# Kernel tuning notes

Hardware: AMD Instinct MI355X
Metric: run time of the kernel (lower is better)

The kernel has to match this reference:

```python
import jax, jax.numpy as jnp
import numpy as np

PAST = 12
FUTURE = 12
INPUT_SIZE = 256
OUTPUT_SIZE = FUTURE * INPUT_SIZE  # 3072


def setup_inputs() -> dict:
    key = jax.random.key(0)
    k_inp, k_w, k_b = jax.random.split(key, 3)
    inp = jax.random.normal(k_inp, (64, 288, INPUT_SIZE), dtype=jnp.float32)
    fan_in = INPUT_SIZE * PAST
    bound = 1.0 / np.sqrt(fan_in)
    # torch nn.Linear init: U(-1/sqrt(fan_in), 1/sqrt(fan_in)); W is (out, in)
    W = jax.random.uniform(k_w, (OUTPUT_SIZE, fan_in), minval=-bound, maxval=bound, dtype=jnp.float32)
    b = jax.random.uniform(k_b, (OUTPUT_SIZE,), minval=-bound, maxval=bound, dtype=jnp.float32)
    return {"inp": inp, "W": W, "b": b}


def reference(inp, W, b):
    batch, length, dim = inp.shape
    n_win = length - PAST  # number of sliding windows (torch loop count)
    # Gather all overlapping windows at once: (batch, n_win, PAST, dim)
    idx = jnp.arange(n_win)[:, None] + jnp.arange(PAST)[None, :]
    windows = inp[:, idx, :].reshape(batch, n_win, PAST * dim)
    # One batched GEMM replaces n_win tiny Linear calls: x @ W.T + b
    out = jnp.einsum('bnk,ok->bno', windows, W) + b
    return out.reshape(batch, -1, FUTURE, dim)
```

## Files before the change

### kernel.cpp

```cpp
#include <hip/hip_runtime.h>
#include <hip/hip_bf16.h>

#define BATCH   64
#define LEN     288
#define DIM     256
#define PAST    12
#define NWIN    (LEN - PAST)
#define M_DIM   (BATCH * NWIN)
#define K_DIM   (PAST * DIM)
#define N_DIM   3072

#define BM 256
#define BN 256
#define BK 64
#define NTILE   (K_DIM / BK)
#define NITER   (NTILE / 2)

#define GRID_N   12
#define BULK_WG  768
#define TAIL_M0  16384
#define TAIL_QN  24
#define TAIL_WG  240

typedef __attribute__((ext_vector_type(8))) short bh8;
typedef __attribute__((ext_vector_type(4))) float f32x4;

__device__ __forceinline__ void llds16(const void* g, void* l) {
    __builtin_amdgcn_global_load_lds(
        (const __attribute__((address_space(1))) unsigned int*)g,
        (__attribute__((address_space(3))) unsigned int*)l,
        16, 0, 0);
}

__global__ void cvt_f32_bf16(const float* __restrict__ in,
                             __hip_bfloat16* __restrict__ out, int n8) {
    int i = blockIdx.x * blockDim.x + threadIdx.x;
    if (i >= n8) return;
    const float4* p = (const float4*)in;
    float4 a = p[2 * i], b = p[2 * i + 1];
    union { __hip_bfloat16 h[8]; int4 v; } u;
    u.h[0] = __float2bfloat16(a.x); u.h[1] = __float2bfloat16(a.y);
    u.h[2] = __float2bfloat16(a.z); u.h[3] = __float2bfloat16(a.w);
    u.h[4] = __float2bfloat16(b.x); u.h[5] = __float2bfloat16(b.y);
    u.h[6] = __float2bfloat16(b.z); u.h[7] = __float2bfloat16(b.w);
    ((int4*)out)[i] = u.v;
}

#define PH_MID  __builtin_amdgcn_sched_barrier(0); __builtin_amdgcn_s_barrier(); \
                __builtin_amdgcn_sched_barrier(0); __builtin_amdgcn_s_setprio(1);
#define PH_END  __builtin_amdgcn_s_setprio(0); __builtin_amdgcn_sched_barrier(0); \
                __builtin_amdgcn_s_barrier(); __builtin_amdgcn_sched_barrier(0);
#define PH_END_VM(N) __builtin_amdgcn_s_setprio(0); __builtin_amdgcn_sched_barrier(0); \
                asm volatile("s_waitcnt vmcnt(" #N ")" ::: "memory"); \
                __builtin_amdgcn_s_barrier(); __builtin_amdgcn_sched_barrier(0);

#define LDS_A(buf) (smem + (buf) * 65536)
#define LDS_B(buf) (smem + (buf) * 65536 + 32768)

#define RD_A4(buf, MB) { \
    const char* _b = LDS_A(buf) + aRowB; \
    _Pragma("unroll") for (int mi = 0; mi < 4; ++mi) { \
        a0[mi][0] = *(const bh8*)(_b + (MB + mi) * 2048 + kOff0); \
        a0[mi][1] = *(const bh8*)(_b + (MB + mi) * 2048 + kOff1); \
    } }
#define RD_B2(buf, dst, NB) { \
    const char* _b = LDS_B(buf) + bRowB; \
    _Pragma("unroll") for (int ni = 0; ni < 2; ++ni) { \
        dst[ni][0] = *(const bh8*)(_b + (NB + ni) * 2048 + kOff0); \
        dst[ni][1] = *(const bh8*)(_b + (NB + ni) * 2048 + kOff1); \
    } }
#define MFMA_Q(MB, NB, BB) \
    _Pragma("unroll") for (int mi = 0; mi < 4; ++mi) \
    _Pragma("unroll") for (int ni = 0; ni < 2; ++ni) { \
        acc[MB + mi][NB + ni] = __builtin_amdgcn_mfma_f32_16x16x32_bf16( \
            a0[mi][0], BB[ni][0], acc[MB + mi][NB + ni], 0, 0, 0); \
        acc[MB + mi][NB + ni] = __builtin_amdgcn_mfma_f32_16x16x32_bf16( \
            a0[mi][1], BB[ni][1], acc[MB + mi][NB + ni], 0, 0, 0); \
    }
#define STG_A1(buf, kt, q) \
    llds16(Ag + aSrc[q] + (kt) * 64, LDS_A(buf) + (q) * 8192 + wOff);
#define STG_B1(buf, kt, u) \
    llds16(Wg + bSrc[u] + (kt) * 64, LDS_B(buf) + (u) * 8192 + wOff);

__global__ __launch_bounds__(512, 2)
void gemm_bulk(const __hip_bfloat16* __restrict__ Ag,
               const __hip_bfloat16* __restrict__ Wg,
               const float* __restrict__ bias,
               float* __restrict__ C)
{
    extern __shared__ char smem[];

    const int tid = threadIdx.x;
    const int wgid = (blockIdx.x & 7) * (BULK_WG / 8) + (blockIdx.x >> 3);
    const int bm = wgid / GRID_N;
    const int bn = wgid - bm * GRID_N;
    const int tile_m = bm * BM;
    const int tile_n = bn * BN;

    const int rd  = tid >> 3;
    const int chs = (((tid & 7) ^ (rd & 7)) * 8);
    int aSrc[4], bSrc[4];
#pragma unroll
    for (int rb = 0; rb < 4; ++rb) {
        int m  = tile_m + rb * 64 + rd;
        int bq = m / NWIN;
        int wq = m - bq * NWIN;
        aSrc[rb] = (bq * LEN + wq) * DIM + chs;
        bSrc[rb] = (tile_n + rb * 64 + rd) * K_DIM + chs;
    }

    const int wave = tid >> 6, lane = tid & 63;
    const int wm = wave >> 2, wn = wave & 3;
    const int fr = lane & 15, kg = lane >> 4;
    const int sw    = (fr & 7) << 4;
    const int kOff0 = (kg * 16) ^ sw;
    const int kOff1 = kOff0 ^ 64;
    const int aRowB = (wm * 128 + fr) * 128;
    const int bRowB = (wn * 64 + fr) * 128;
    const int wOff  = wave * 1024;

    bh8 a0[4][2], fb0[2][2], fb1[2][2];
    f32x4 acc[8][4] = {};

    STG_A1(0, 0, 0); STG_A1(0, 0, 1); STG_A1(0, 0, 2); STG_A1(0, 0, 3);
    STG_B1(0, 0, 0); STG_B1(0, 0, 1); STG_B1(0, 0, 2); STG_B1(0, 0, 3);
    STG_A1(1, 1, 0); STG_A1(1, 1, 2);
    STG_B1(1, 1, 0); STG_B1(1, 1, 1);
    STG_A1(1, 1, 1); STG_A1(1, 1, 3);
    asm volatile("s_waitcnt vmcnt(6)" ::: "memory");
    __builtin_amdgcn_s_barrier();
    __builtin_amdgcn_sched_barrier(0);

#pragma unroll 1
    for (int it = 0; it < NITER; ++it) {
        const int b = 2 * it + 1;
        int c = 2 * it + 2; if (c >= NTILE) c = NTILE - 2;
        int d = 2 * it + 3; if (d >= NTILE) d = NTILE - 1;

        RD_B2(0, fb0, 0); RD_A4(0, 0);
        STG_B1(1, b, 2); STG_B1(1, b, 3);
        PH_MID; MFMA_Q(0, 0, fb0); PH_END;

        RD_B2(0, fb1, 2);
        STG_A1(0, c, 0); STG_A1(0, c, 2);
        PH_MID; MFMA_Q(0, 2, fb1); PH_END;

        RD_A4(0, 4);
        STG_B1(0, c, 0); STG_B1(0, c, 1);
        PH_MID; MFMA_Q(4, 2, fb1); PH_END;

        STG_A1(0, c, 1); STG_A1(0, c, 3);
        PH_MID; MFMA_Q(4, 0, fb0); PH_END_VM(6);

        RD_B2(1, fb0, 0); RD_A4(1, 0);
        STG_B1(0, c, 2); STG_B1(0, c, 3);
        PH_MID; MFMA_Q(0, 0, fb0); PH_END;

        RD_B2(1, fb1, 2);
        STG_A1(1, d, 0); STG_A1(1, d, 2);
        PH_MID; MFMA_Q(0, 2, fb1); PH_END;

        RD_A4(1, 4);
        STG_B1(1, d, 0); STG_B1(1, d, 1);
        PH_MID; MFMA_Q(4, 2, fb1); PH_END;

        STG_A1(1, d, 1); STG_A1(1, d, 3);
        PH_MID; MFMA_Q(4, 0, fb0); PH_END_VM(6);
    }

    float bv[4];
    const float* bp = bias + tile_n + wn * 64 + fr;
#pragma unroll
    for (int ni = 0; ni < 4; ++ni) bv[ni] = bp[ni * 16];

    const int r0 = (lane >> 4) * 4;
#pragma unroll
    for (int mi = 0; mi < 8; ++mi) {
#pragma unroll
        for (int j = 0; j < 4; ++j) {
            long m = tile_m + wm * 128 + mi * 16 + r0 + j;
            float* crow = C + m * (long)N_DIM + tile_n + wn * 64 + fr;
#pragma unroll
            for (int ni = 0; ni < 4; ++ni)
                __builtin_nontemporal_store(acc[mi][ni][j] + bv[ni], &crow[ni * 16]);
        }
    }
}

#define TLDS_A(buf) (smem + (buf) * 32768)
#define TLDS_B(buf) (smem + (buf) * 32768 + 16384)

#define T_RD(buf) { \
    const char* _bb = TLDS_B(buf) + bRowB; \
    _Pragma("unroll") for (int ni = 0; ni < 2; ++ni) { \
        fb0[ni][0] = *(const bh8*)(_bb + ni * 2048 + kOff0); \
        fb0[ni][1] = *(const bh8*)(_bb + ni * 2048 + kOff1); \
    } \
    const char* _a = TLDS_A(buf) + aRowB; \
    _Pragma("unroll") for (int mi = 0; mi < 4; ++mi) { \
        a0[mi][0] = *(const bh8*)(_a + mi * 2048 + kOff0); \
        a0[mi][1] = *(const bh8*)(_a + mi * 2048 + kOff1); \
    } }
#define T_MFMA(MB) \
    _Pragma("unroll") for (int mi = 0; mi < 2; ++mi) \
    _Pragma("unroll") for (int ni = 0; ni < 2; ++ni) { \
        acc[MB + mi][ni] = __builtin_amdgcn_mfma_f32_16x16x32_bf16( \
            a0[MB + mi][0], fb0[ni][0], acc[MB + mi][ni], 0, 0, 0); \
        acc[MB + mi][ni] = __builtin_amdgcn_mfma_f32_16x16x32_bf16( \
            a0[MB + mi][1], fb0[ni][1], acc[MB + mi][ni], 0, 0, 0); \
    }
#define T_STG_A(buf, kt, u) \
    llds16(Ag + aSrc[u] + (kt) * 64, TLDS_A(buf) + (u) * 8192 + wOff);
#define T_STG_B(buf, kt, u) \
    llds16(Wg + bSrc[u] + (kt) * 64, TLDS_B(buf) + (u) * 8192 + wOff);

__global__ __launch_bounds__(512, 2)
void gemm_tail(const __hip_bfloat16* __restrict__ Ag,
               const __hip_bfloat16* __restrict__ Wg,
               const float* __restrict__ bias,
               float* __restrict__ C)
{
    extern __shared__ char smem[];

    const int tid = threadIdx.x;
    const int wgid = (blockIdx.x & 7) * (TAIL_WG / 8) + (blockIdx.x >> 3);
    const int qm = wgid / TAIL_QN;
    const int qn = wgid - qm * TAIL_QN;
    const int tile_m = TAIL_M0 + qm * 128;
    const int tile_n = qn * 128;

    const int rd  = tid >> 3;
    const int chs = (((tid & 7) ^ (rd & 7)) * 8);
    int aSrc[2], bSrc[2];
#pragma unroll
    for (int rb = 0; rb < 2; ++rb) {
        int m  = tile_m + rb * 64 + rd;
        int bq = m / NWIN;
        int wq = m - bq * NWIN;
        aSrc[rb] = (bq * LEN + wq) * DIM + chs;
        bSrc[rb] = (tile_n + rb * 64 + rd) * K_DIM + chs;
    }

    const int wave = tid >> 6, lane = tid & 63;
    const int wm = wave >> 2, wn = wave & 3;
    const int fr = lane & 15, kg = lane >> 4;
    const int sw    = (fr & 7) << 4;
    const int kOff0 = (kg * 16) ^ sw;
    const int kOff1 = kOff0 ^ 64;
    const int aRowB = (wm * 64 + fr) * 128;
    const int bRowB = (wn * 32 + fr) * 128;
    const int wOff  = wave * 1024;

    bh8 a0[4][2], fb0[2][2];
    f32x4 acc[4][2] = {};

    T_STG_A(0, 0, 0); T_STG_A(0, 0, 1); T_STG_B(0, 0, 0); T_STG_B(0, 0, 1);
    T_STG_A(1, 1, 0); T_STG_A(1, 1, 1);
    asm volatile("s_waitcnt vmcnt(2)" ::: "memory");
    __builtin_amdgcn_s_barrier();
    __builtin_amdgcn_sched_barrier(0);

#pragma unroll 1
    for (int it = 0; it < NITER; ++it) {
        const int b = 2 * it + 1;
        int c = 2 * it + 2; if (c >= NTILE) c = NTILE - 2;
        int d = 2 * it + 3; if (d >= NTILE) d = NTILE - 1;

        T_RD(0);
        T_STG_B(1, b, 0); T_STG_B(1, b, 1);
        PH_MID; T_MFMA(0); PH_END;

        T_STG_A(0, c, 0); T_STG_A(0, c, 1);
        PH_MID; T_MFMA(2); PH_END_VM(2);

        T_RD(1);
        T_STG_B(0, c, 0); T_STG_B(0, c, 1);
        PH_MID; T_MFMA(0); PH_END;

        T_STG_A(1, d, 0); T_STG_A(1, d, 1);
        PH_MID; T_MFMA(2); PH_END_VM(2);
    }

    float bv[2];
    const float* bp = bias + tile_n + wn * 32 + fr;
#pragma unroll
    for (int ni = 0; ni < 2; ++ni) bv[ni] = bp[ni * 16];

    const int r0 = (lane >> 4) * 4;
#pragma unroll
    for (int mi = 0; mi < 4; ++mi) {
#pragma unroll
        for (int j = 0; j < 4; ++j) {
            long m = tile_m + wm * 64 + mi * 16 + r0 + j;
            float* crow = C + m * (long)N_DIM + tile_n + wn * 32 + fr;
#pragma unroll
            for (int ni = 0; ni < 2; ++ni)
                __builtin_nontemporal_store(acc[mi][ni][j] + bv[ni], &crow[ni * 16]);
        }
    }
}

extern "C" void kernel_launch(void* const* d_in, const int* in_sizes, int n_in,
                              void* d_out, int out_size, void* d_ws, size_t ws_size,
                              hipStream_t stream) {
    const float* inp  = (const float*)d_in[0];
    const float* Wf   = (const float*)d_in[1];
    const float* bias = (const float*)d_in[2];
    float* out = (float*)d_out;

    __hip_bfloat16* Abf = (__hip_bfloat16*)d_ws;
    __hip_bfloat16* Wbf = (__hip_bfloat16*)((char*)d_ws + (size_t)BATCH * LEN * DIM * 2);

    const int nA8 = BATCH * LEN * DIM / 8;
    const int nW8 = N_DIM * K_DIM / 8;
    cvt_f32_bf16<<<(nA8 + 255) / 256, 256, 0, stream>>>(inp, Abf, nA8);
    cvt_f32_bf16<<<(nW8 + 255) / 256, 256, 0, stream>>>(Wf, Wbf, nW8);

    hipFuncSetAttribute((const void*)gemm_bulk,
                        hipFuncAttributeMaxDynamicSharedMemorySize, 131072);
    hipFuncSetAttribute((const void*)gemm_tail,
                        hipFuncAttributeMaxDynamicSharedMemorySize, 65536);
    gemm_bulk<<<dim3(BULK_WG), 512, 131072, stream>>>(Abf, Wbf, bias, out);
    gemm_tail<<<dim3(TAIL_WG), 512, 65536, stream>>>(Abf, Wbf, bias, out);
}
```

Measured before the change: 308.4 us.

## Software-pipeline LDS fragment reads one phase ahead by splitting along K

Restructures the bulk GEMM main loop so each phase computes a full 4x4 MFMA quadrant for one K half, with A/B fragments double-buffered in registers (aP/aQ, bP/bQ) and loaded one phase ahead of use. This hides LDS read latency behind the MFMAs of the previous phase. The vmcnt wait moves earlier, to the third phase, with a smaller count. The change raises register pressure, risks reading the next LDS buffer before it is fully ready, and adds an extra prefetch at the loop tail that reads buffer 0 after the final iteration.

Result: no change. 308.1 us (-0.1%).

```diff
diff --git a/kernel.cpp b/kernel.cpp
--- a/kernel.cpp
+++ b/kernel.cpp
@@ -57,26 +57,19 @@
 #define LDS_A(buf) (smem + (buf) * 65536)
 #define LDS_B(buf) (smem + (buf) * 65536 + 32768)
 
-#define RD_A4(buf, MB) { \
+#define RD_AK(buf, MB, KO, dst) { \
     const char* _b = LDS_A(buf) + aRowB; \
-    _Pragma("unroll") for (int mi = 0; mi < 4; ++mi) { \
-        a0[mi][0] = *(const bh8*)(_b + (MB + mi) * 2048 + kOff0); \
-        a0[mi][1] = *(const bh8*)(_b + (MB + mi) * 2048 + kOff1); \
-    } }
-#define RD_B2(buf, dst, NB) { \
+    _Pragma("unroll") for (int mi = 0; mi < 4; ++mi) \
+        dst[mi] = *(const bh8*)(_b + ((MB) + mi) * 2048 + (KO)); }
+#define RD_BK(buf, KO, dst) { \
     const char* _b = LDS_B(buf) + bRowB; \
-    _Pragma("unroll") for (int ni = 0; ni < 2; ++ni) { \
-        dst[ni][0] = *(const bh8*)(_b + (NB + ni) * 2048 + kOff0); \
-        dst[ni][1] = *(const bh8*)(_b + (NB + ni) * 2048 + kOff1); \
-    } }
-#define MFMA_Q(MB, NB, BB) \
+    _Pragma("unroll") for (int ni = 0; ni < 4; ++ni) \
+        dst[ni] = *(const bh8*)(_b + ni * 2048 + (KO)); }
+#define MFMA_K(MB, AS, BS) \
     _Pragma("unroll") for (int mi = 0; mi < 4; ++mi) \
-    _Pragma("unroll") for (int ni = 0; ni < 2; ++ni) { \
-        acc[MB + mi][NB + ni] = __builtin_amdgcn_mfma_f32_16x16x32_bf16( \
-            a0[mi][0], BB[ni][0], acc[MB + mi][NB + ni], 0, 0, 0); \
-        acc[MB + mi][NB + ni] = __builtin_amdgcn_mfma_f32_16x16x32_bf16( \
-            a0[mi][1], BB[ni][1], acc[MB + mi][NB + ni], 0, 0, 0); \
-    }
+    _Pragma("unroll") for (int ni = 0; ni < 4; ++ni) \
+        acc[(MB) + mi][ni] = __builtin_amdgcn_mfma_f32_16x16x32_bf16( \
+            AS[mi], BS[ni], acc[(MB) + mi][ni], 0, 0, 0);
 #define STG_A1(buf, kt, q) \
     llds16(Ag + aSrc[q] + (kt) * 64, LDS_A(buf) + (q) * 8192 + wOff);
 #define STG_B1(buf, kt, u) \
@@ -119,7 +112,7 @@
     const int bRowB = (wn * 64 + fr) * 128;
     const int wOff  = wave * 1024;
 
-    bh8 a0[4][2], fb0[2][2], fb1[2][2];
+    bh8 aP[4], aQ[4], bP[4], bQ[4];
     f32x4 acc[8][4] = {};
 
     STG_A1(0, 0, 0); STG_A1(0, 0, 1); STG_A1(0, 0, 2); STG_A1(0, 0, 3);
@@ -131,41 +124,45 @@
     __builtin_amdgcn_s_barrier();
     __builtin_amdgcn_sched_barrier(0);
 
+    RD_AK(0, 0, kOff0, aP); RD_BK(0, kOff0, bP);
+
 #pragma unroll 1
     for (int it = 0; it < NITER; ++it) {
         const int b = 2 * it + 1;
         int c = 2 * it + 2; if (c >= NTILE) c = NTILE - 2;
         int d = 2 * it + 3; if (d >= NTILE) d = NTILE - 1;
 
-        RD_B2(0, fb0, 0); RD_A4(0, 0);
+        RD_AK(0, 0, kOff1, aQ); RD_BK(0, kOff1, bQ);
         STG_B1(1, b, 2); STG_B1(1, b, 3);
-        PH_MID; MFMA_Q(0, 0, fb0); PH_END;
-
-        RD_B2(0, fb1, 2);
+        PH_MID; MFMA_K(0, aP, bP); PH_END;
+
+        RD_AK(0, 4, kOff0, aP);
         STG_A1(0, c, 0); STG_A1(0, c, 2);
-        PH_MID; MFMA_Q(0, 2, fb1); PH_END;
-
-        RD_A4(0, 4);
+        PH_MID; MFMA_K(0, aQ, bQ); PH_END;
+
+        RD_AK(0, 4, kOff1, aQ);
         STG_B1(0, c, 0); STG_B1(0, c, 1);
-        PH_MID; MFMA_Q(4, 2, fb1); PH_END;
-
+        PH_MID; MFMA_K(4, aP, bP); PH_END_VM(4);
+
+        RD_AK(1, 0, kOff0, aP); RD_BK(1, kOff0, bP);
         STG_A1(0, c, 1); STG_A1(0, c, 3);
-        PH_MID; MFMA_Q(4, 0, fb0); PH_END_VM(6);
-
-        RD_B2(1, fb0, 0); RD_A4(1, 0);
+        PH_MID; MFMA_K(4, aQ, bQ); PH_END;
+
+        RD_AK(1, 0, kOff1, aQ); RD_BK(1, kOff1, bQ);
         STG_B1(0, c, 2); STG_B1(0, c, 3);
-        PH_MID; MFMA_Q(0, 0, fb0); PH_END;
-
-        RD_B2(1, fb1, 2);
+        PH_MID; MFMA_K(0, aP, bP); PH_END;
+
+        RD_AK(1, 4, kOff0, aP);
         STG_A1(1, d, 0); STG_A1(1, d, 2);
-        PH_MID; MFMA_Q(0, 2, fb1); PH_END;
-
-        RD_A4(1, 4);
+        PH_MID; MFMA_K(0, aQ, bQ); PH_END;
+
+        RD_AK(1, 4, kOff1, aQ);
         STG_B1(1, d, 0); STG_B1(1, d, 1);
-        PH_MID; MFMA_Q(4, 2, fb1); PH_END;
-
+        PH_MID; MFMA_K(4, aP, bP); PH_END_VM(4);
+
+        RD_AK(0, 0, kOff0, aP); RD_BK(0, kOff0, bP);
         STG_A1(1, d, 1); STG_A1(1, d, 3);
-        PH_MID; MFMA_Q(4, 0, fb0); PH_END_VM(6);
+        PH_MID; MFMA_K(4, aQ, bQ); PH_END;
     }
 
     float bv[4];
```
